# Kernel optimization log

Measured on AMD Instinct MI355X. Metric: run time of the kernel, lower is better.

The kernel has to match this reference:

```python
import jax, jax.numpy as jnp
import numpy as np

B, N, D = 2, 4096, 1024
DS = 1024           # state_dim (defaults to embed_dim)
H = 4096            # mlp hidden = int(embed_dim * 4.0)
EPS = 1e-5


def _layernorm(x, w, b):
    mu = jnp.mean(x, axis=-1, keepdims=True)
    var = jnp.mean((x - mu) ** 2, axis=-1, keepdims=True)
    return (x - mu) * jax.lax.rsqrt(var + EPS) * w + b


def _selective_scan(deltaA, deltaB_u):
    # deltaA: (B, N, 1), deltaB_u: (B, N, DS). Recurrence h_i = dA_i * h + dBu_i.
    def step(h, inp):
        dA, dBu = inp           # (B,1), (B,DS)
        h = dA * h + dBu
        return h, h
    h0 = jnp.zeros((deltaB_u.shape[0], deltaB_u.shape[2]), deltaB_u.dtype)
    _, ys = jax.lax.scan(step, h0,
                         (jnp.swapaxes(deltaA, 0, 1), jnp.swapaxes(deltaB_u, 0, 1)))
    return jnp.swapaxes(ys, 0, 1)   # (B, N, DS)


def _forward(x, norm1_w, norm1_b, gate_w, gate_b, state_w, state_b,
             out_w, out_b, norm2_w, norm2_b, mlp_w1, mlp_b1, mlp_w2, mlp_b2):
    xn = _layernorm(x, norm1_w, norm1_b)
    g = xn @ gate_w + gate_b                       # (B,N,2D)
    gate, gate_gate = jnp.split(g, 2, axis=-1)
    gate = jax.nn.silu(gate)
    gate_gate = jax.nn.silu(gate_gate)
    u = (xn * gate) @ state_w + state_b            # (B,N,DS)
    Bm = gate_gate @ state_w + state_b             # (B,N,DS)
    # A = -ones(DS) -> delta*A = -delta broadcast over DS; keep (B,N,1)
    delta = jax.nn.softplus(jnp.mean(xn @ state_w + state_b, axis=-1, keepdims=True))
    deltaA = jnp.exp(-delta)                       # (B,N,1)
    deltaB_u = delta * Bm * u                      # (B,N,DS)
    # C = ones -> y_i = C_i * h_i = h_i
    y = _selective_scan(deltaA, deltaB_u)
    ssm_out = y @ out_w + out_b
    x = x + ssm_out
    x2 = _layernorm(x, norm2_w, norm2_b)
    mlp = jax.nn.gelu(x2 @ mlp_w1 + mlp_b1, approximate=False) @ mlp_w2 + mlp_b2
    return x + mlp


def setup_inputs() -> dict:
    key = jax.random.key(0)
    ks = jax.random.split(key, 12)
    s = 0.02
    p = lambda k, shape: jax.random.normal(k, shape, jnp.float32) * s
    return {
        "x": jax.random.normal(ks[0], (B, N, D), jnp.float32),
        "norm1_w": jnp.ones((D,), jnp.float32), "norm1_b": jnp.zeros((D,), jnp.float32),
        "gate_w": p(ks[1], (D, 2 * D)), "gate_b": p(ks[2], (2 * D,)),
        "state_w": p(ks[3], (D, DS)), "state_b": p(ks[4], (DS,)),
        "out_w": p(ks[5], (DS, D)), "out_b": p(ks[6], (D,)),
        "norm2_w": jnp.ones((D,), jnp.float32), "norm2_b": jnp.zeros((D,), jnp.float32),
        "mlp_w1": p(ks[7], (D, H)), "mlp_b1": p(ks[8], (H,)),
        "mlp_w2": p(ks[9], (H, D)), "mlp_b2": p(ks[10], (D,)),
    }


def reference(x, norm1_w, norm1_b, gate_w, gate_b, state_w, state_b,
              out_w, out_b, norm2_w, norm2_b, mlp_w1, mlp_b1, mlp_w2, mlp_b2):
    return _forward(x, norm1_w, norm1_b, gate_w, gate_b, state_w, state_b,
                    out_w, out_b, norm2_w, norm2_b, mlp_w1, mlp_b1, mlp_w2, mlp_b2)
```

## Files before the change

kernel.cpp:

```cpp
#include <hip/hip_runtime.h>
#include <hip/hip_bf16.h>
#include <math.h>

#define B_   2
#define N_   4096
#define D_   1024
#define DS_  1024
#define HID_ 4096
#define ROWS (B_ * N_)

#define CHK 128
#define TCH 32

typedef __attribute__((ext_vector_type(8))) short bf16x8;
typedef __attribute__((ext_vector_type(4))) float f32x4;

#define ASG __attribute__((address_space(1)))
#define AS3 __attribute__((address_space(3)))

__device__ __forceinline__ float bf2f(unsigned short u) {
  union { float f; unsigned int i; } v; v.i = ((unsigned int)u) << 16; return v.f;
}
__device__ __forceinline__ unsigned short f2bf(float f) {
  union { float f; unsigned int i; } v; v.f = f;
  unsigned int r = v.i + 0x7fffu + ((v.i >> 16) & 1u);
  return (unsigned short)(r >> 16);
}

__global__ void means_kernel(const float* __restrict__ W, const float* __restrict__ bvec,
                             float* __restrict__ swmean, float* __restrict__ sbmean) {
  __shared__ float sm[4];
  int bid = blockIdx.x, t = threadIdx.x;
  const float* src = (bid < D_) ? (W + (size_t)bid * DS_) : bvec;
  float s = 0.f;
  for (int j = t; j < DS_; j += 256) s += src[j];
  for (int o = 32; o; o >>= 1) s += __shfl_down(s, o);
  if ((t & 63) == 0) sm[t >> 6] = s;
  __syncthreads();
  if (t == 0) {
    float r = (sm[0] + sm[1] + sm[2] + sm[3]) * (1.f / DS_);
    if (bid < D_) swmean[bid] = r; else sbmean[0] = r;
  }
}

__global__ void transpose_bf16_kernel(const float* __restrict__ W, unsigned short* __restrict__ WT,
                                      int K, int N) {
  __shared__ float tile[32][33];
  int tx = threadIdx.x & 31, ty = threadIdx.x >> 5;
  int bn = blockIdx.x * 32, bk = blockIdx.y * 32;
  for (int i = ty; i < 32; i += 8)
    tile[i][tx] = W[(size_t)(bk + i) * N + bn + tx];
  __syncthreads();
  for (int i = ty; i < 32; i += 8)
    WT[(size_t)(bn + i) * K + bk + tx] = f2bf(tile[tx][i]);
}

template<bool WITH_DELTA>
__global__ void ln_kernel(const float* __restrict__ x, const float* __restrict__ w,
                          const float* __restrict__ bb, unsigned short* __restrict__ out_bf,
                          const float* __restrict__ swmean, const float* __restrict__ sbmean,
                          float* __restrict__ delta) {
  __shared__ float sm[8];
  __shared__ float bc[2];
  int row = blockIdx.x, t = threadIdx.x;
  const float* xr = x + (size_t)row * D_;
  float4 xv = ((const float4*)xr)[t];
  float s  = xv.x + xv.y + xv.z + xv.w;
  float sq = xv.x * xv.x + xv.y * xv.y + xv.z * xv.z + xv.w * xv.w;
  for (int o = 32; o; o >>= 1) { s += __shfl_down(s, o); sq += __shfl_down(sq, o); }
  if ((t & 63) == 0) { sm[t >> 6] = s; sm[4 + (t >> 6)] = sq; }
  __syncthreads();
  if (t == 0) {
    float ts = sm[0] + sm[1] + sm[2] + sm[3];
    float tq = sm[4] + sm[5] + sm[6] + sm[7];
    float mu = ts * (1.f / D_);
    float var = tq * (1.f / D_) - mu * mu;
    bc[0] = mu; bc[1] = rsqrtf(var + 1e-5f);
  }
  __syncthreads();
  float mu = bc[0], rs = bc[1];
  float4 wv = ((const float4*)w)[t];
  float4 bv = ((const float4*)bb)[t];
  float n0 = (xv.x - mu) * rs * wv.x + bv.x;
  float n1 = (xv.y - mu) * rs * wv.y + bv.y;
  float n2 = (xv.z - mu) * rs * wv.z + bv.z;
  float n3 = (xv.w - mu) * rs * wv.w + bv.w;
  ushort4 o4; o4.x = f2bf(n0); o4.y = f2bf(n1); o4.z = f2bf(n2); o4.w = f2bf(n3);
  ((ushort4*)(out_bf + (size_t)row * D_))[t] = o4;
  if (WITH_DELTA) {
    float4 sw = ((const float4*)swmean)[t];
    float d = n0 * sw.x + n1 * sw.y + n2 * sw.z + n3 * sw.w;
    for (int o = 32; o; o >>= 1) d += __shfl_down(d, o);
    if ((t & 63) == 0) sm[t >> 6] = d;
    __syncthreads();
    if (t == 0) {
      float z = sm[0] + sm[1] + sm[2] + sm[3] + sbmean[0];
      delta[row] = (z > 15.f) ? z : log1pf(__expf(z));
    }
  }
}


#define BARX { __builtin_amdgcn_s_barrier(); __builtin_amdgcn_sched_barrier(0); }

#define RD_A(TAU, H) { const char* ab_ = smem + ((((TAU)&1)*2+(H))<<14); \
  _Pragma("unroll") for (int mm_ = 0; mm_ < MB_H; ++mm_) \
  _Pragma("unroll") for (int ks_ = 0; ks_ < 2; ++ks_) { \
    int r_ = wr*(16*MB_H) + mm_*16 + l15; \
    int by_ = r_*128 + ks_*64 + kq16; by_ ^= ((by_>>7)&7)<<4; \
    af[mm_][ks_] = *(const bf16x8*)(ab_ + by_); } }

#define RD_B(TAU, H, DST) { const char* bb_ = smemB + ((((TAU)&1)*2+(H)))*SB; \
  _Pragma("unroll") for (int nn_ = 0; nn_ < NB_H; ++nn_) \
  _Pragma("unroll") for (int ks_ = 0; ks_ < 2; ++ks_) { \
    int r_ = wc*(16*NB_H) + nn_*16 + l15; \
    int by_ = r_*128 + ks_*64 + kq16; by_ ^= ((by_>>7)&7)<<4; \
    DST[nn_][ks_] = *(const bf16x8*)(bb_ + by_); } }

#define MFMAQ(QA, QB, BF) { __builtin_amdgcn_s_setprio(1); \
  _Pragma("unroll") for (int m_ = 0; m_ < MB_H; ++m_) \
  _Pragma("unroll") for (int n_ = 0; n_ < NB_H; ++n_) \
  _Pragma("unroll") for (int k_ = 0; k_ < 2; ++k_) \
    acc[(QA)*MB_H+m_][(QB)*NB_H+n_] = __builtin_amdgcn_mfma_f32_16x16x32_bf16( \
        af[m_][k_], BF[n_][k_], acc[(QA)*MB_H+m_][(QB)*NB_H+n_], 0, 0, 0); \
  __builtin_amdgcn_s_setprio(0); }

template<int BN, int EPI>
__global__ __launch_bounds__(512, 2) void gemm8p(
    const unsigned short* __restrict__ A1p, int lda1, int M1,
    const unsigned short* __restrict__ A2p, int lda2,
    const unsigned short* __restrict__ BT, const float* __restrict__ bias,
    void* __restrict__ Cout, const float* __restrict__ res,
    int N, int K, int nbx) {
  constexpr int WN   = (BN == 256) ? 4 : 2;
  constexpr int MB_H = (BN == 256) ? 4 : 2;
  constexpr int NB_H = 2;
  constexpr int MF   = 2 * MB_H;
  constexpr int LB   = BN / 128;
  constexpr int SB   = (BN / 2) * 64 * 2;
  __shared__ char smem[65536 + 4 * SB];
  char* smemB = smem + 65536;

  const int nwg = gridDim.x;
  int bid = blockIdx.x;
  int wg = (bid & 7) * (nwg >> 3) + (bid >> 3);
  const int bx = wg % nbx, by = wg / nbx;
  const int mbase = by * 256, nbase = bx * BN;

  const int tid = threadIdx.x;
  const int lane = tid & 63, wid = tid >> 6;
  const int wr = wid / WN, wc = wid % WN;
  const int l15 = lane & 15, kq16 = (lane >> 4) * 16;
  const int wvoff16 = wid << 10;

  const unsigned short* Ause; int ldaU;
  if (mbase < M1) { Ause = A1p + (size_t)mbase * lda1; ldaU = lda1; }
  else            { Ause = A2p + (size_t)(mbase - M1) * lda2; ldaU = lda2; }

  int L0 = tid * 16;        int b0 = L0 ^ (((L0 >> 7) & 7) << 4);
  int L1 = 8192 + tid * 16; int b1 = L1 ^ (((L1 >> 7) & 7) << 4);
  const unsigned short* pA0 = Ause + (size_t)(b0 >> 7) * ldaU + ((b0 & 127) >> 1);
  const unsigned short* pA1 = Ause + (size_t)(b1 >> 7) * ldaU + ((b1 & 127) >> 1);
  const unsigned short* pB0 = BT + (size_t)(nbase + (b0 >> 7)) * K + ((b0 & 127) >> 1);
  const unsigned short* pB1 = BT + (size_t)(nbase + (b1 >> 7)) * K + ((b1 & 127) >> 1);

  auto stageA = [&](int tau, int h, bool en) {
    if (!en) return;
    char* l0 = smem + (((tau & 1) * 2 + h) << 14) + wvoff16;
    const unsigned short* g0 = pA0 + (size_t)h * 128 * ldaU + tau * 64;
    const unsigned short* g1 = pA1 + (size_t)h * 128 * ldaU + tau * 64;
    __builtin_amdgcn_global_load_lds((const ASG void*)g0, (AS3 void*)l0, 16, 0, 0);
    __builtin_amdgcn_global_load_lds((const ASG void*)g1, (AS3 void*)(l0 + 8192), 16, 0, 0);
  };
  auto stageB = [&](int tau, int h, bool en) {
    if (!en) return;
    char* l0 = smemB + ((tau & 1) * 2 + h) * SB + wvoff16;
    const unsigned short* g0 = pB0 + (size_t)h * (BN / 2) * K + tau * 64;
    __builtin_amdgcn_global_load_lds((const ASG void*)g0, (AS3 void*)l0, 16, 0, 0);
    if constexpr (LB == 2) {
      const unsigned short* g1 = pB1 + (size_t)h * (BN / 2) * K + tau * 64;
      __builtin_amdgcn_global_load_lds((const ASG void*)g1, (AS3 void*)(l0 + 8192), 16, 0, 0);
    }
  };
  auto vm_steady = [&]() {
    if constexpr (BN == 256) { asm volatile("s_waitcnt vmcnt(6)" ::: "memory"); }
    else                     { asm volatile("s_waitcnt vmcnt(5)" ::: "memory"); }
  };

  f32x4 acc[MF][4];
#pragma unroll
  for (int m = 0; m < MF; ++m)
#pragma unroll
    for (int n = 0; n < 4; ++n) acc[m][n] = (f32x4){0.f, 0.f, 0.f, 0.f};
  bf16x8 af[MB_H][2], bq0[NB_H][2], bq1[NB_H][2];

  const int NT = K >> 6, NI = NT >> 1;

  stageA(0, 0, true); stageB(0, 0, true); stageA(0, 1, true); stageB(0, 1, true);
  stageA(1, 0, true); stageB(1, 0, true); stageA(1, 1, true);
  vm_steady();
  BARX;

#pragma unroll 1
  for (int i = 0; i < NI; ++i) {
    const int t0 = 2 * i;
    const bool st = (i < NI - 1);
    RD_A(t0, 0); RD_B(t0, 0, bq0); stageB(t0 + 1, 1, true);
    BARX; MFMAQ(0, 0, bq0); BARX;
    RD_B(t0, 1, bq1); stageA(t0 + 2, 0, st);
    BARX; MFMAQ(0, 1, bq1); BARX;
    RD_A(t0, 1); stageB(t0 + 2, 0, st);
    BARX; MFMAQ(1, 1, bq1); BARX;
    stageA(t0 + 2, 1, st);
    if (st) { vm_steady(); } else { asm volatile("s_waitcnt vmcnt(0)" ::: "memory"); }
    BARX; MFMAQ(1, 0, bq0); BARX;
    RD_A(t0 + 1, 0); RD_B(t0 + 1, 0, bq0); stageB(t0 + 2, 1, st);
    BARX; MFMAQ(0, 0, bq0); BARX;
    RD_B(t0 + 1, 1, bq1); stageA(t0 + 3, 0, st);
    BARX; MFMAQ(0, 1, bq1); BARX;
    RD_A(t0 + 1, 1); stageB(t0 + 3, 0, st);
    BARX; MFMAQ(1, 1, bq1); BARX;
    stageA(t0 + 3, 1, st);
    if (st) vm_steady();
    BARX; MFMAQ(1, 0, bq0); BARX;
  }

#pragma unroll
  for (int mb = 0; mb < MF; ++mb) {
    int row = mbase + wr * (16 * MB_H) + (mb % MB_H) * 16 + (mb / MB_H) * 128 + (lane >> 4) * 4;
#pragma unroll
    for (int nb = 0; nb < 4; ++nb) {
      int col = nbase + wc * (16 * NB_H) + (nb % NB_H) * 16 + (nb / NB_H) * (BN / 2) + l15;
      float bc = bias[col];
#pragma unroll
      for (int r = 0; r < 4; ++r) {
        float v = acc[mb][nb][r] + bc;
        size_t off = (size_t)(row + r) * N + col;
        if (EPI == 1) {
          v = v / (1.f + __expf(-v));
          ((unsigned short*)Cout)[off] = f2bf(v);
        } else if (EPI == 2) {
          ((unsigned short*)Cout)[off] = f2bf(v);
        } else if (EPI == 3) {
          ((float*)Cout)[off] = v + res[off];
        } else if (EPI == 4) {
          float tt = v * (0.7978845608f + 0.0356774081f * v * v);
          v = v / (1.f + __expf(-2.f * tt));
          ((unsigned short*)Cout)[off] = f2bf(v);
        }
      }
    }
  }
}

__global__ void ew_xg_kernel(const unsigned short* __restrict__ xn,
                             const unsigned short* __restrict__ gs,
                             unsigned short* __restrict__ xg) {
  size_t i8 = ((size_t)blockIdx.x * 256 + threadIdx.x) * 8;
  size_t row = i8 >> 10, col = i8 & 1023;
  uint4 xv = *(const uint4*)(xn + i8);
  uint4 gv = *(const uint4*)(gs + row * 2048 + col);
  const unsigned short* xs = (const unsigned short*)&xv;
  const unsigned short* gg = (const unsigned short*)&gv;
  uint4 ov; unsigned short* o = (unsigned short*)&ov;
#pragma unroll
  for (int j = 0; j < 8; ++j) o[j] = f2bf(bf2f(xs[j]) * bf2f(gg[j]));
  *(uint4*)(xg + i8) = ov;
}

__global__ void ew_dbu_kernel(const unsigned short* __restrict__ u,
                              const unsigned short* __restrict__ bm,
                              const float* __restrict__ delta,
                              unsigned short* __restrict__ dbu) {
  size_t i8 = ((size_t)blockIdx.x * 256 + threadIdx.x) * 8;
  size_t row = i8 >> 10;
  float dl = delta[row];
  uint4 uv = *(const uint4*)(u + i8);
  uint4 bv = *(const uint4*)(bm + i8);
  const unsigned short* us = (const unsigned short*)&uv;
  const unsigned short* bs = (const unsigned short*)&bv;
  uint4 ov; unsigned short* o = (unsigned short*)&ov;
#pragma unroll
  for (int j = 0; j < 8; ++j) o[j] = f2bf(dl * bf2f(us[j]) * bf2f(bs[j]));
  *(uint4*)(dbu + i8) = ov;
}

__global__ void scan_a_kernel(const unsigned short* __restrict__ dbu,
                              const float* __restrict__ delta,
                              float* __restrict__ hend, float* __restrict__ S) {
  int blk = blockIdx.x;
  int b = blk / CHK, c = blk % CHK;
  int ch = threadIdx.x;
  const unsigned short* p = dbu + ((size_t)(b * N_ + c * TCH)) * DS_ + ch;
  const float* dp = delta + b * N_ + c * TCH;
  float h = 0.f, dsum = 0.f;
#pragma unroll 4
  for (int t = 0; t < TCH; ++t) {
    float dl = dp[t];
    h = __expf(-dl) * h + bf2f(p[(size_t)t * DS_]);
    dsum += dl;
  }
  hend[(size_t)blk * DS_ + ch] = h;
  if (ch == 0) S[blk] = dsum;
}

__global__ void scan_combine_kernel(const float* __restrict__ hend, const float* __restrict__ S,
                                    float* __restrict__ carryin) {
  int b = blockIdx.x, ch = threadIdx.x;
  float carry = 0.f;
  for (int c = 0; c < CHK; ++c) {
    size_t o = (size_t)(b * CHK + c) * DS_ + ch;
    carryin[o] = carry;
    carry = __expf(-S[b * CHK + c]) * carry + hend[o];
  }
}

__global__ void scan_b_kernel(const unsigned short* __restrict__ dbu,
                              const float* __restrict__ delta,
                              const float* __restrict__ carryin,
                              unsigned short* __restrict__ y) {
  int blk = blockIdx.x;
  int b = blk / CHK, c = blk % CHK;
  int ch = threadIdx.x;
  size_t base = ((size_t)(b * N_ + c * TCH)) * DS_ + ch;
  const float* dp = delta + b * N_ + c * TCH;
  float h = carryin[(size_t)blk * DS_ + ch];
#pragma unroll 4
  for (int t = 0; t < TCH; ++t) {
    h = __expf(-dp[t]) * h + bf2f(dbu[base + (size_t)t * DS_]);
    y[base + (size_t)t * DS_] = f2bf(h);
  }
}

extern "C" void kernel_launch(void* const* d_in, const int* in_sizes, int n_in,
                              void* d_out, int out_size, void* d_ws, size_t ws_size,
                              hipStream_t stream) {
  const float* x       = (const float*)d_in[0];
  const float* n1w     = (const float*)d_in[1];
  const float* n1b     = (const float*)d_in[2];
  const float* gate_w  = (const float*)d_in[3];
  const float* gate_b  = (const float*)d_in[4];
  const float* state_w = (const float*)d_in[5];
  const float* state_b = (const float*)d_in[6];
  const float* out_w   = (const float*)d_in[7];
  const float* out_b   = (const float*)d_in[8];
  const float* n2w     = (const float*)d_in[9];
  const float* n2b     = (const float*)d_in[10];
  const float* mlp_w1  = (const float*)d_in[11];
  const float* mlp_b1  = (const float*)d_in[12];
  const float* mlp_w2  = (const float*)d_in[13];
  const float* mlp_b2  = (const float*)d_in[14];
  float* outp = (float*)d_out;

  char* w = (char*)d_ws;
  size_t off = 0;
  auto alloc = [&](size_t bytes) { char* p = w + off; off += (bytes + 255) & ~(size_t)255; return p; };

  unsigned short* gate_wT  = (unsigned short*)alloc((size_t)2048 * 1024 * 2);
  unsigned short* state_wT = (unsigned short*)alloc((size_t)1024 * 1024 * 2);
  unsigned short* out_wT   = (unsigned short*)alloc((size_t)1024 * 1024 * 2);
  unsigned short* w1T      = (unsigned short*)alloc((size_t)4096 * 1024 * 2);
  unsigned short* w2T      = (unsigned short*)alloc((size_t)1024 * 4096 * 2);
  float* swmean  = (float*)alloc(D_ * 4);
  float* sbmean  = (float*)alloc(256);
  float* delta   = (float*)alloc((size_t)ROWS * 4);
  float* hend    = (float*)alloc((size_t)B_ * CHK * DS_ * 4);
  float* carryin = (float*)alloc((size_t)B_ * CHK * DS_ * 4);
  float* S       = (float*)alloc((size_t)B_ * CHK * 4);
  unsigned short* xn = (unsigned short*)alloc((size_t)ROWS * D_ * 2);
  unsigned short* gs = (unsigned short*)alloc((size_t)ROWS * HID_ * 2);
  unsigned short* xg = (unsigned short*)alloc((size_t)ROWS * D_ * 2);
  float* x1          = (float*)alloc((size_t)ROWS * D_ * 4);

  unsigned short* dbu = xn;
  unsigned short* h1  = gs;
  unsigned short* y   = xg;
  unsigned short* x2  = xg;
  unsigned short* u   = (unsigned short*)x1;
  unsigned short* bm  = u + (size_t)ROWS * D_;

  means_kernel<<<D_ + 1, 256, 0, stream>>>(state_w, state_b, swmean, sbmean);
  transpose_bf16_kernel<<<dim3(2048 / 32, 1024 / 32), 256, 0, stream>>>(gate_w, gate_wT, 1024, 2048);
  transpose_bf16_kernel<<<dim3(1024 / 32, 1024 / 32), 256, 0, stream>>>(state_w, state_wT, 1024, 1024);
  transpose_bf16_kernel<<<dim3(1024 / 32, 1024 / 32), 256, 0, stream>>>(out_w, out_wT, 1024, 1024);
  transpose_bf16_kernel<<<dim3(4096 / 32, 1024 / 32), 256, 0, stream>>>(mlp_w1, w1T, 1024, 4096);
  transpose_bf16_kernel<<<dim3(1024 / 32, 4096 / 32), 256, 0, stream>>>(mlp_w2, w2T, 4096, 1024);

  ln_kernel<true><<<ROWS, 256, 0, stream>>>(x, n1w, n1b, xn, swmean, sbmean, delta);

  const int BIG = 1 << 30;
  gemm8p<256, 1><<<256, 512, 0, stream>>>(xn, 1024, BIG, xn, 1024,
                                          gate_wT, gate_b, gs, nullptr, 2048, 1024, 8);
  ew_xg_kernel<<<(ROWS * D_) / 8 / 256, 256, 0, stream>>>(xn, gs, xg);
  gemm8p<256, 2><<<256, 512, 0, stream>>>(xg, 1024, 8192, gs + 1024, 2048,
                                          state_wT, state_b, u, nullptr, 1024, 1024, 4);
  ew_dbu_kernel<<<(ROWS * D_) / 8 / 256, 256, 0, stream>>>(u, bm, delta, dbu);

  scan_a_kernel<<<B_ * CHK, 1024, 0, stream>>>(dbu, delta, hend, S);
  scan_combine_kernel<<<B_, 1024, 0, stream>>>(hend, S, carryin);
  scan_b_kernel<<<B_ * CHK, 1024, 0, stream>>>(dbu, delta, carryin, y);

  gemm8p<128, 3><<<256, 512, 0, stream>>>(y, 1024, BIG, y, 1024,
                                          out_wT, out_b, x1, x, 1024, 1024, 8);
  ln_kernel<false><<<ROWS, 256, 0, stream>>>(x1, n2w, n2b, x2, nullptr, nullptr, nullptr);
  gemm8p<256, 4><<<512, 512, 0, stream>>>(x2, 1024, BIG, x2, 1024,
                                          w1T, mlp_b1, h1, nullptr, 4096, 1024, 16);
  gemm8p<128, 3><<<256, 512, 0, stream>>>(h1, 4096, BIG, h1, 4096,
                                          w2T, mlp_b2, outp, x1, 1024, 4096, 8);
}
```

Before: 367.4 us.

## Fuse dBu product into scan kernels, merge weight transposes, precompute exp(-delta)

Drops the separate elementwise kernel that built delta*Bm*u. Both scan passes now read u and Bm directly and form the product inline, which removes one write and one read of a large bf16 tensor. The five weight transposes become a single launch, and exp(-delta) is computed once in the layernorm kernel so the scans reuse it, with chunk carries using a product of decays instead of exp of a sum. The GEMM main loop also issues global stage loads before the LDS fragment reads. In exchange, both scan passes read two input tensors instead of one.

```diff
diff --git a/kernel.cpp b/kernel.cpp
--- a/kernel.cpp
+++ b/kernel.cpp
@@ -43,11 +43,23 @@
   }
 }
 
-__global__ void transpose_bf16_kernel(const float* __restrict__ W, unsigned short* __restrict__ WT,
-                                      int K, int N) {
+__global__ void transpose_all_kernel(const float* __restrict__ gw, const float* __restrict__ sw,
+                                     const float* __restrict__ ow, const float* __restrict__ w1,
+                                     const float* __restrict__ w2,
+                                     unsigned short* __restrict__ gwT, unsigned short* __restrict__ swT,
+                                     unsigned short* __restrict__ owT, unsigned short* __restrict__ w1T,
+                                     unsigned short* __restrict__ w2T) {
   __shared__ float tile[32][33];
+  int b = blockIdx.x;
+  const float* W; unsigned short* WT; int K, N, t0;
+  if (b < 2048)      { W = gw; WT = gwT; K = 1024; N = 2048; t0 = b; }
+  else if (b < 3072) { W = sw; WT = swT; K = 1024; N = 1024; t0 = b - 2048; }
+  else if (b < 4096) { W = ow; WT = owT; K = 1024; N = 1024; t0 = b - 3072; }
+  else if (b < 8192) { W = w1; WT = w1T; K = 1024; N = 4096; t0 = b - 4096; }
+  else               { W = w2; WT = w2T; K = 4096; N = 1024; t0 = b - 8192; }
+  int ntx = N >> 5;
+  int bn = (t0 % ntx) * 32, bk = (t0 / ntx) * 32;
   int tx = threadIdx.x & 31, ty = threadIdx.x >> 5;
-  int bn = blockIdx.x * 32, bk = blockIdx.y * 32;
   for (int i = ty; i < 32; i += 8)
     tile[i][tx] = W[(size_t)(bk + i) * N + bn + tx];
   __syncthreads();
@@ -59,7 +71,7 @@
 __global__ void ln_kernel(const float* __restrict__ x, const float* __restrict__ w,
                           const float* __restrict__ bb, unsigned short* __restrict__ out_bf,
                           const float* __restrict__ swmean, const float* __restrict__ sbmean,
-                          float* __restrict__ delta) {
+                          float* __restrict__ delta, float* __restrict__ ea) {
   __shared__ float sm[8];
   __shared__ float bc[2];
   int row = blockIdx.x, t = threadIdx.x;
@@ -95,7 +107,9 @@
     __syncthreads();
     if (t == 0) {
       float z = sm[0] + sm[1] + sm[2] + sm[3] + sbmean[0];
-      delta[row] = (z > 15.f) ? z : log1pf(__expf(z));
+      float dl = (z > 15.f) ? z : log1pf(__expf(z));
+      delta[row] = dl;
+      ea[row] = __expf(-dl);
     }
   }
 }
@@ -205,29 +219,30 @@
   for (int i = 0; i < NI; ++i) {
     const int t0 = 2 * i;
     const bool st = (i < NI - 1);
-    RD_A(t0, 0); RD_B(t0, 0, bq0); stageB(t0 + 1, 1, true);
+    stageB(t0 + 1, 1, true); RD_A(t0, 0); RD_B(t0, 0, bq0);
     BARX; MFMAQ(0, 0, bq0); BARX;
-    RD_B(t0, 1, bq1); stageA(t0 + 2, 0, st);
+    stageA(t0 + 2, 0, st); RD_B(t0, 1, bq1);
     BARX; MFMAQ(0, 1, bq1); BARX;
-    RD_A(t0, 1); stageB(t0 + 2, 0, st);
+    stageB(t0 + 2, 0, st); RD_A(t0, 1);
     BARX; MFMAQ(1, 1, bq1); BARX;
     stageA(t0 + 2, 1, st);
     if (st) { vm_steady(); } else { asm volatile("s_waitcnt vmcnt(0)" ::: "memory"); }
     BARX; MFMAQ(1, 0, bq0); BARX;
-    RD_A(t0 + 1, 0); RD_B(t0 + 1, 0, bq0); stageB(t0 + 2, 1, st);
+    stageB(t0 + 2, 1, st); RD_A(t0 + 1, 0); RD_B(t0 + 1, 0, bq0);
     BARX; MFMAQ(0, 0, bq0); BARX;
-    RD_B(t0 + 1, 1, bq1); stageA(t0 + 3, 0, st);
+    stageA(t0 + 3, 0, st); RD_B(t0 + 1, 1, bq1);
     BARX; MFMAQ(0, 1, bq1); BARX;
-    RD_A(t0 + 1, 1); stageB(t0 + 3, 0, st);
+    stageB(t0 + 3, 0, st); RD_A(t0 + 1, 1);
     BARX; MFMAQ(1, 1, bq1); BARX;
     stageA(t0 + 3, 1, st);
     if (st) vm_steady();
     BARX; MFMAQ(1, 0, bq0); BARX;
   }
 
+  const int r0 = (lane >> 4) * 4;
 #pragma unroll
   for (int mb = 0; mb < MF; ++mb) {
-    int row = mbase + wr * (16 * MB_H) + (mb % MB_H) * 16 + (mb / MB_H) * 128 + (lane >> 4) * 4;
+    int row = mbase + wr * (16 * MB_H) + (mb % MB_H) * 16 + (mb / MB_H) * 128 + r0;
 #pragma unroll
     for (int nb = 0; nb < 4; ++nb) {
       int col = nbase + wc * (16 * NB_H) + (nb % NB_H) * 16 + (nb / NB_H) * (BN / 2) + l15;
@@ -268,55 +283,44 @@
   *(uint4*)(xg + i8) = ov;
 }
 
-__global__ void ew_dbu_kernel(const unsigned short* __restrict__ u,
+__global__ void scan_a_kernel(const unsigned short* __restrict__ u,
                               const unsigned short* __restrict__ bm,
                               const float* __restrict__ delta,
-                              unsigned short* __restrict__ dbu) {
-  size_t i8 = ((size_t)blockIdx.x * 256 + threadIdx.x) * 8;
-  size_t row = i8 >> 10;
-  float dl = delta[row];
-  uint4 uv = *(const uint4*)(u + i8);
-  uint4 bv = *(const uint4*)(bm + i8);
-  const unsigned short* us = (const unsigned short*)&uv;
-  const unsigned short* bs = (const unsigned short*)&bv;
-  uint4 ov; unsigned short* o = (unsigned short*)&ov;
-#pragma unroll
-  for (int j = 0; j < 8; ++j) o[j] = f2bf(dl * bf2f(us[j]) * bf2f(bs[j]));
-  *(uint4*)(dbu + i8) = ov;
-}
-
-__global__ void scan_a_kernel(const unsigned short* __restrict__ dbu,
-                              const float* __restrict__ delta,
-                              float* __restrict__ hend, float* __restrict__ S) {
+                              const float* __restrict__ ea,
+                              float* __restrict__ hend, float* __restrict__ P) {
   int blk = blockIdx.x;
   int b = blk / CHK, c = blk % CHK;
   int ch = threadIdx.x;
-  const unsigned short* p = dbu + ((size_t)(b * N_ + c * TCH)) * DS_ + ch;
+  size_t base = ((size_t)(b * N_ + c * TCH)) * DS_ + ch;
   const float* dp = delta + b * N_ + c * TCH;
-  float h = 0.f, dsum = 0.f;
+  const float* ep = ea + b * N_ + c * TCH;
+  float h = 0.f, pa = 1.f;
 #pragma unroll 4
   for (int t = 0; t < TCH; ++t) {
-    float dl = dp[t];
-    h = __expf(-dl) * h + bf2f(p[(size_t)t * DS_]);
-    dsum += dl;
+    float dl = dp[t], e = ep[t];
+    float du = dl * bf2f(u[base + (size_t)t * DS_]) * bf2f(bm[base + (size_t)t * DS_]);
+    h = e * h + du;
+    pa *= e;
   }
   hend[(size_t)blk * DS_ + ch] = h;
-  if (ch == 0) S[blk] = dsum;
-}
-
-__global__ void scan_combine_kernel(const float* __restrict__ hend, const float* __restrict__ S,
+  if (ch == 0) P[blk] = pa;
+}
+
+__global__ void scan_combine_kernel(const float* __restrict__ hend, const float* __restrict__ P,
                                     float* __restrict__ carryin) {
   int b = blockIdx.x, ch = threadIdx.x;
   float carry = 0.f;
   for (int c = 0; c < CHK; ++c) {
     size_t o = (size_t)(b * CHK + c) * DS_ + ch;
     carryin[o] = carry;
-    carry = __expf(-S[b * CHK + c]) * carry + hend[o];
-  }
-}
-
-__global__ void scan_b_kernel(const unsigned short* __restrict__ dbu,
+    carry = P[b * CHK + c] * carry + hend[o];
+  }
+}
+
+__global__ void scan_b_kernel(const unsigned short* __restrict__ u,
+                              const unsigned short* __restrict__ bm,
                               const float* __restrict__ delta,
+                              const float* __restrict__ ea,
                               const float* __restrict__ carryin,
                               unsigned short* __restrict__ y) {
   int blk = blockIdx.x;
@@ -324,10 +328,13 @@
   int ch = threadIdx.x;
   size_t base = ((size_t)(b * N_ + c * TCH)) * DS_ + ch;
   const float* dp = delta + b * N_ + c * TCH;
+  const float* ep = ea + b * N_ + c * TCH;
   float h = carryin[(size_t)blk * DS_ + ch];
 #pragma unroll 4
   for (int t = 0; t < TCH; ++t) {
-    h = __expf(-dp[t]) * h + bf2f(dbu[base + (size_t)t * DS_]);
+    float dl = dp[t], e = ep[t];
+    float du = dl * bf2f(u[base + (size_t)t * DS_]) * bf2f(bm[base + (size_t)t * DS_]);
+    h = e * h + du;
     y[base + (size_t)t * DS_] = f2bf(h);
   }
 }
@@ -364,29 +371,26 @@
   float* swmean  = (float*)alloc(D_ * 4);
   float* sbmean  = (float*)alloc(256);
   float* delta   = (float*)alloc((size_t)ROWS * 4);
+  float* eadel   = (float*)alloc((size_t)ROWS * 4);
   float* hend    = (float*)alloc((size_t)B_ * CHK * DS_ * 4);
   float* carryin = (float*)alloc((size_t)B_ * CHK * DS_ * 4);
-  float* S       = (float*)alloc((size_t)B_ * CHK * 4);
+  float* P       = (float*)alloc((size_t)B_ * CHK * 4);
   unsigned short* xn = (unsigned short*)alloc((size_t)ROWS * D_ * 2);
   unsigned short* gs = (unsigned short*)alloc((size_t)ROWS * HID_ * 2);
   unsigned short* xg = (unsigned short*)alloc((size_t)ROWS * D_ * 2);
   float* x1          = (float*)alloc((size_t)ROWS * D_ * 4);
 
-  unsigned short* dbu = xn;
-  unsigned short* h1  = gs;
-  unsigned short* y   = xg;
-  unsigned short* x2  = xg;
-  unsigned short* u   = (unsigned short*)x1;
-  unsigned short* bm  = u + (size_t)ROWS * D_;
+  unsigned short* h1 = gs;
+  unsigned short* y  = xg;
+  unsigned short* x2 = xg;
+  unsigned short* u  = (unsigned short*)x1;
+  unsigned short* bm = u + (size_t)ROWS * D_;
 
   means_kernel<<<D_ + 1, 256, 0, stream>>>(state_w, state_b, swmean, sbmean);
-  transpose_bf16_kernel<<<dim3(2048 / 32, 1024 / 32), 256, 0, stream>>>(gate_w, gate_wT, 1024, 2048);
-  transpose_bf16_kernel<<<dim3(1024 / 32, 1024 / 32), 256, 0, stream>>>(state_w, state_wT, 1024, 1024);
-  transpose_bf16_kernel<<<dim3(1024 / 32, 1024 / 32), 256, 0, stream>>>(out_w, out_wT, 1024, 1024);
-  transpose_bf16_kernel<<<dim3(4096 / 32, 1024 / 32), 256, 0, stream>>>(mlp_w1, w1T, 1024, 4096);
-  transpose_bf16_kernel<<<dim3(1024 / 32, 4096 / 32), 256, 0, stream>>>(mlp_w2, w2T, 4096, 1024);
-
-  ln_kernel<true><<<ROWS, 256, 0, stream>>>(x, n1w, n1b, xn, swmean, sbmean, delta);
+  transpose_all_kernel<<<12288, 256, 0, stream>>>(gate_w, state_w, out_w, mlp_w1, mlp_w2,
+                                                  gate_wT, state_wT, out_wT, w1T, w2T);
+
+  ln_kernel<true><<<ROWS, 256, 0, stream>>>(x, n1w, n1b, xn, swmean, sbmean, delta, eadel);
 
   const int BIG = 1 << 30;
   gemm8p<256, 1><<<256, 512, 0, stream>>>(xn, 1024, BIG, xn, 1024,
@@ -394,15 +398,14 @@
   ew_xg_kernel<<<(ROWS * D_) / 8 / 256, 256, 0, stream>>>(xn, gs, xg);
   gemm8p<256, 2><<<256, 512, 0, stream>>>(xg, 1024, 8192, gs + 1024, 2048,
                                           state_wT, state_b, u, nullptr, 1024, 1024, 4);
-  ew_dbu_kernel<<<(ROWS * D_) / 8 / 256, 256, 0, stream>>>(u, bm, delta, dbu);
-
-  scan_a_kernel<<<B_ * CHK, 1024, 0, stream>>>(dbu, delta, hend, S);
-  scan_combine_kernel<<<B_, 1024, 0, stream>>>(hend, S, carryin);
-  scan_b_kernel<<<B_ * CHK, 1024, 0, stream>>>(dbu, delta, carryin, y);
+
+  scan_a_kernel<<<B_ * CHK, 1024, 0, stream>>>(u, bm, delta, eadel, hend, P);
+  scan_combine_kernel<<<B_, 1024, 0, stream>>>(hend, P, carryin);
+  scan_b_kernel<<<B_ * CHK, 1024, 0, stream>>>(u, bm, delta, eadel, carryin, y);
 
   gemm8p<128, 3><<<256, 512, 0, stream>>>(y, 1024, BIG, y, 1024,
                                           out_wT, out_b, x1, x, 1024, 1024, 8);
-  ln_kernel<false><<<ROWS, 256, 0, stream>>>(x1, n2w, n2b, x2, nullptr, nullptr, nullptr);
+  ln_kernel<false><<<ROWS, 256, 0, stream>>>(x1, n2w, n2b, x2, nullptr, nullptr, nullptr, nullptr);
   gemm8p<256, 4><<<512, 512, 0, stream>>>(x2, 1024, BIG, x2, 1024,
                                           w1T, mlp_b1, h1, nullptr, 4096, 1024, 16);
   gemm8p<128, 3><<<256, 512, 0, stream>>>(h1, 4096, BIG, h1, 4096,
```

After: 355.8 us. -3.2%, faster.
